# Kernel optimization log

Hardware: AMD Instinct MI355X
Metric: run time of the kernel (lower is better)

Reference implementation:

```python
import jax, jax.numpy as jnp
import numpy as np

B, N, D = 2, 2048, 1024
H, DH = 16, 64
DEPTH = 4
FF = 4
EPS = 1e-3  # keras LayerNormalization default epsilon
SCALE = DH ** -0.5


def setup_inputs() -> dict:
    key = jax.random.key(0)
    ks = jax.random.split(key, 8)
    s = 0.02
    inner = H * DH
    return {
        "x": jax.random.normal(ks[0], (B, N, D), jnp.float32),
        "mask": jnp.ones((B, N), jnp.bool_),
        "ln1_g": jnp.ones((DEPTH, D), jnp.float32),
        "ln1_b": jnp.zeros((DEPTH, D), jnp.float32),
        "Wqkv": jax.random.normal(ks[1], (DEPTH, D, 3 * inner), jnp.float32) * s,
        "Wout": jax.random.normal(ks[2], (DEPTH, inner, D), jnp.float32) * s,
        "bout": jnp.zeros((DEPTH, D), jnp.float32),
        "ln2_g": jnp.ones((DEPTH, D), jnp.float32),
        "ln2_b": jnp.zeros((DEPTH, D), jnp.float32),
        "W1": jax.random.normal(ks[3], (DEPTH, D, 2 * FF * D), jnp.float32) * s,
        "b1": jnp.zeros((DEPTH, 2 * FF * D), jnp.float32),
        "W2": jax.random.normal(ks[4], (DEPTH, FF * D, D), jnp.float32) * s,
        "b2": jnp.zeros((DEPTH, D), jnp.float32),
    }


def _layernorm(x, g, b):
    mu = jnp.mean(x, axis=-1, keepdims=True)
    var = jnp.mean(jnp.square(x - mu), axis=-1, keepdims=True)
    return (x - mu) * jax.lax.rsqrt(var + EPS) * g + b


def _attention(x, mask, Wqkv, Wout, bout):
    b, n, _ = x.shape
    qkv = x @ Wqkv  # [b, n, 3*h*dh]
    q, k, v = jnp.split(qkv, 3, axis=-1)
    split_heads = lambda t: t.reshape(b, n, H, DH).transpose(0, 2, 1, 3)  # b h n d
    q, k, v = split_heads(q), split_heads(k), split_heads(v)
    dots = jnp.einsum("bhid,bhjd->bhij", q, k) * SCALE
    neg = -jnp.finfo(dots.dtype).max
    # padding mask: keep (i valid) & (j valid)
    pm = mask[:, None, :, None] & mask[:, None, None, :]
    dots = jnp.where(pm, dots, neg)
    # causal mask: strict upper triangle masked out (triu with k=1)
    causal = jnp.triu(jnp.ones((n, n), jnp.bool_), k=1)
    dots = jnp.where(causal, neg, dots)
    attn = jax.nn.softmax(dots, axis=-1)
    out = jnp.einsum("bhij,bhjd->bhid", attn, v)
    out = out.transpose(0, 2, 1, 3).reshape(b, n, H * DH)
    return out @ Wout + bout


def _feedforward(x, W1, b1, W2, b2):
    h = x @ W1 + b1
    a, gates = jnp.split(h, 2, axis=-1)
    h = a * jax.nn.gelu(gates, approximate=False)  # GEGLU, tf.nn.gelu exact
    return h @ W2 + b2


def reference(x, mask, ln1_g, ln1_b, Wqkv, Wout, bout, ln2_g, ln2_b, W1, b1, W2, b2):
    for l in range(DEPTH):
        x = x + _attention(_layernorm(x, ln1_g[l], ln1_b[l]), mask, Wqkv[l], Wout[l], bout[l])
        x = x + _feedforward(_layernorm(x, ln2_g[l], ln2_b[l]), W1[l], b1[l], W2[l], b2[l])
    return x
```

## Files before the change

### kernel.cpp

```cpp
#include <hip/hip_runtime.h>


typedef float f32x4 __attribute__((ext_vector_type(4)));
typedef __bf16 bf16x8 __attribute__((ext_vector_type(8)));
typedef unsigned short u16;
typedef unsigned int u32;

#define SCALE2 0.18033688011112042f
#define LN_EPS 1e-3f
#define DEFER_THR 8.0f

__device__ __forceinline__ float fexp2(float x) { return __builtin_amdgcn_exp2f(x); }

__device__ __forceinline__ u16 f2bf(float f) {
  u32 u = __float_as_uint(f);
  u += 0x7fffu + ((u >> 16) & 1u);
  return (u16)(u >> 16);
}

__device__ __forceinline__ void stage16(void* lds_wave_base, const void* gsrc) {
  __builtin_amdgcn_global_load_lds((__attribute__((address_space(1))) void*)gsrc,
                                   (__attribute__((address_space(3))) void*)lds_wave_base,
                                   16, 0, 0);
}

__global__ void wtrans_kernel(const float* __restrict__ W, u16* __restrict__ WT,
                              int K, int N, int permMode) {
  __shared__ float tile[32][33];
  const int n0 = blockIdx.x * 32, k0 = blockIdx.y * 32;
  const float* Wl = W + (size_t)blockIdx.z * K * N;
  u16* WTl = WT + (size_t)blockIdx.z * K * N;
  const int tx = threadIdx.x, ty = threadIdx.y;
#pragma unroll
  for (int i = 0; i < 4; ++i)
    tile[ty + i * 8][tx] = Wl[(size_t)(k0 + ty + i * 8) * N + n0 + tx];
  __syncthreads();
#pragma unroll
  for (int i = 0; i < 4; ++i) {
    const int n = n0 + ty + i * 8;
    int orow;
    if (permMode) {
      orow = (n < 4096) ? (((n >> 4) << 5) + (n & 15))
                        : ((((n - 4096) >> 4) << 5) + 16 + (n & 15));
    } else {
      orow = n;
    }
    WTl[(size_t)orow * K + k0 + tx] = f2bf(tile[tx][ty + i * 8]);
  }
}

__global__ void vtrans_kernel(const u16* __restrict__ qkv, u16* __restrict__ Vt) {
  __shared__ u16 tile[32][33];
  const int t0 = blockIdx.x * 32, d0 = blockIdx.y * 32, bh = blockIdx.z;
  const int b = bh >> 4, h = bh & 15;
  const int tx = threadIdx.x, ty = threadIdx.y;
#pragma unroll
  for (int i = 0; i < 4; ++i)
    tile[ty + i * 8][tx] =
        qkv[((size_t)(b * 2048 + t0 + ty + i * 8)) * 3072 + 2048 + h * 64 + d0 + tx];
  __syncthreads();
#pragma unroll
  for (int i = 0; i < 4; ++i)
    Vt[((size_t)bh * 64 + d0 + ty + i * 8) * 2048 + t0 + tx] = tile[tx][ty + i * 8];
}

__global__ __launch_bounds__(256, 4)
void ln_kernel(const float* __restrict__ x, const float* __restrict__ g,
               const float* __restrict__ b, u16* __restrict__ y) {
  const int row = blockIdx.x, tid = threadIdx.x;
  const float4 v = ((const float4*)(x + (size_t)row * 1024))[tid];
  float s = v.x + v.y + v.z + v.w;
  float s2 = v.x * v.x + v.y * v.y + v.z * v.z + v.w * v.w;
#pragma unroll
  for (int off = 32; off > 0; off >>= 1) {
    s += __shfl_down(s, off);
    s2 += __shfl_down(s2, off);
  }
  __shared__ float ps[8];
  __shared__ float stats[2];
  const int wv = tid >> 6, lane = tid & 63;
  if (lane == 0) { ps[wv] = s; ps[wv + 4] = s2; }
  __syncthreads();
  if (tid == 0) {
    const float S = ps[0] + ps[1] + ps[2] + ps[3];
    const float S2 = ps[4] + ps[5] + ps[6] + ps[7];
    const float mu = S * (1.0f / 1024.0f);
    const float var = S2 * (1.0f / 1024.0f) - mu * mu;
    stats[0] = mu;
    stats[1] = rsqrtf(var + LN_EPS);
  }
  __syncthreads();
  const float mu = stats[0], rs = stats[1];
  const float4 gg = ((const float4*)g)[tid];
  const float4 bb = ((const float4*)b)[tid];
  ushort4 ov;
  ov.x = f2bf((v.x - mu) * rs * gg.x + bb.x);
  ov.y = f2bf((v.y - mu) * rs * gg.y + bb.y);
  ov.z = f2bf((v.z - mu) * rs * gg.z + bb.z);
  ov.w = f2bf((v.w - mu) * rs * gg.w + bb.w);
  ((ushort4*)(y + (size_t)row * 1024))[tid] = ov;
}

template <int EPI, int BM, int BN, int WM, int WN>
__global__ __launch_bounds__(WM * WN * 64, 2)
void gemm4(const u16* __restrict__ A, const u16* __restrict__ B,
           float* __restrict__ resid, const float* __restrict__ bias,
           u16* __restrict__ out, int M, int N, int K) {
  constexpr int NTHR = WM * WN * 64;
  constexpr int MT = BM / WM / 16;
  constexpr int NT = BN / WN / 16;
  __shared__ __align__(16) u16 lds[2][(BM + BN) * 64];

  const int tid = threadIdx.x;
  const int wv = tid >> 6, lane = tid & 63;
  const int lr = lane & 15, lg = lane >> 4;
  const int wmi = wv / WN, wni = wv % WN;
  const int RB0 = wmi * (BM / WM), CB0 = wni * (BN / WN);

  const int nwg = (int)(gridDim.x * gridDim.y);
  int id = (int)(blockIdx.y * gridDim.x + blockIdx.x);
  id = (id & 7) * (nwg >> 3) + (id >> 3);
  const int m0 = (id / (int)gridDim.x) * BM, n0 = (id % (int)gridDim.x) * BN;

  auto stage = [&](int bsel, int k0) {
    u16* dstA = &lds[bsel][0];
    u16* dstB = &lds[bsel][BM * 64];
#pragma unroll
    for (int rnd = 0; rnd < (BM * 128) / (NTHR * 16); ++rnd) {
      const int base = rnd * (NTHR * 16) + wv * 1024;
      const int off = base + lane * 16;
      const int row = off >> 7;
      const int k2 = (off & 127) ^ ((row & 7) << 4);
      stage16((char*)dstA + base, A + (size_t)(m0 + row) * K + k0 + (k2 >> 1));
    }
#pragma unroll
    for (int rnd = 0; rnd < (BN * 128) / (NTHR * 16); ++rnd) {
      const int base = rnd * (NTHR * 16) + wv * 1024;
      const int off = base + lane * 16;
      const int row = off >> 7;
      const int k2 = (off & 127) ^ ((row & 7) << 4);
      stage16((char*)dstB + base, B + (size_t)(n0 + row) * K + k0 + (k2 >> 1));
    }
  };

  f32x4 acc[MT][NT] = {};
  bf16x8 afr0[MT], bfr0[NT], afr1[MT], bfr1[NT];

  auto rd = [&](int bsel, int ks, bf16x8 (&af)[MT], bf16x8 (&bf)[NT]) {
    const char* As = (const char*)&lds[bsel][0];
    const char* Bs = (const char*)&lds[bsel][BM * 64];
#pragma unroll
    for (int mt = 0; mt < MT; ++mt) {
      const int row = RB0 + mt * 16 + lr;
      af[mt] = *(const bf16x8*)(As + row * 128 + ((ks * 64 + lg * 16) ^ ((lr & 7) << 4)));
    }
#pragma unroll
    for (int nt = 0; nt < NT; ++nt) {
      const int row = CB0 + nt * 16 + lr;
      bf[nt] = *(const bf16x8*)(Bs + row * 128 + ((ks * 64 + lg * 16) ^ ((lr & 7) << 4)));
    }
  };

  const int nT = K >> 6;
  stage(0, 0);
  stage(1, 64);
  asm volatile("s_waitcnt vmcnt(8)\n\ts_barrier" ::: "memory");
  rd(0, 0, afr0, bfr0);
  __builtin_amdgcn_sched_barrier(0);

  for (int t = 0; t < nT; ++t) {
    const int c = t & 1;
    rd(c, 1, afr1, bfr1);
    __builtin_amdgcn_sched_barrier(0);
    __builtin_amdgcn_s_setprio(1);
#pragma unroll
    for (int mt = 0; mt < MT; ++mt)
#pragma unroll
      for (int nt = 0; nt < NT; ++nt)
        acc[mt][nt] = __builtin_amdgcn_mfma_f32_16x16x32_bf16(
            afr0[mt], bfr0[nt], acc[mt][nt], 0, 0, 0);
    __builtin_amdgcn_s_setprio(0);
    __builtin_amdgcn_sched_barrier(0);
    asm volatile("s_waitcnt lgkmcnt(0)\n\ts_barrier" ::: "memory");
    __builtin_amdgcn_sched_barrier(0);
    if (t + 2 < nT) stage(c, (t + 2) * 64);
    if (t + 1 < nT) {
      if (t + 2 < nT)
        asm volatile("s_waitcnt vmcnt(8)\n\ts_barrier" ::: "memory");
      else
        asm volatile("s_waitcnt vmcnt(0)\n\ts_barrier" ::: "memory");
      rd(c ^ 1, 0, afr0, bfr0);
      __builtin_amdgcn_sched_barrier(0);
    }
    __builtin_amdgcn_s_setprio(1);
#pragma unroll
    for (int mt = 0; mt < MT; ++mt)
#pragma unroll
      for (int nt = 0; nt < NT; ++nt)
        acc[mt][nt] = __builtin_amdgcn_mfma_f32_16x16x32_bf16(
            afr1[mt], bfr1[nt], acc[mt][nt], 0, 0, 0);
    __builtin_amdgcn_s_setprio(0);
  }

  if (EPI == 0) {
#pragma unroll
    for (int mt = 0; mt < MT; ++mt)
#pragma unroll
      for (int nt = 0; nt < NT; ++nt) {
        const int n = n0 + CB0 + nt * 16 + lr;
#pragma unroll
        for (int r = 0; r < 4; ++r) {
          const int m = m0 + RB0 + mt * 16 + lg * 4 + r;
          out[(size_t)m * N + n] = f2bf(acc[mt][nt][r]);
        }
      }
  } else if (EPI == 1) {
    float bs[NT];
#pragma unroll
    for (int nt = 0; nt < NT; ++nt) bs[nt] = bias[n0 + CB0 + nt * 16 + lr];
#pragma unroll
    for (int mt = 0; mt < MT; ++mt)
#pragma unroll
      for (int nt = 0; nt < NT; ++nt) {
        const int n = n0 + CB0 + nt * 16 + lr;
#pragma unroll
        for (int r = 0; r < 4; ++r) {
          const int m = m0 + RB0 + mt * 16 + lg * 4 + r;
          resid[(size_t)m * N + n] += acc[mt][nt][r] + bs[nt];
        }
      }
  } else {
#pragma unroll
    for (int pt = 0; pt < NT / 2; ++pt) {
      const int colA = ((n0 + CB0 + pt * 32) >> 5) * 16 + lr;
      const float ba = bias[colA];
      const float bg = bias[4096 + colA];
#pragma unroll
      for (int mt = 0; mt < MT; ++mt)
#pragma unroll
        for (int r = 0; r < 4; ++r) {
          const int m = m0 + RB0 + mt * 16 + lg * 4 + r;
          const float a = acc[mt][2 * pt][r] + ba;
          const float g = acc[mt][2 * pt + 1][r] + bg;
          const float gl = 0.5f * g * (1.0f + erff(g * 0.70710678118654752f));
          out[(size_t)m * 4096 + colA] = f2bf(a * gl);
        }
    }
  }
}

__global__ __launch_bounds__(512, 4)
void attn_kernel(const u16* __restrict__ qkv, const u16* __restrict__ Vt,
                 u16* __restrict__ attnout) {
  __shared__ __align__(16) u16 KV[2][2][64 * 64];
  __shared__ __align__(16) u16 Ps[8][16 * 64];

  const int tid = threadIdx.x;
  const int wv = tid >> 6, lane = tid & 63;
  const int lr = lane & 15, lg = lane >> 4;
  const int lin = (int)(blockIdx.y * gridDim.x + blockIdx.x);
  const int xcd = lin & 7, j = lin >> 3;
  const int bh = xcd * 4 + (j >> 4);
  const int pr = j & 15;
  const int b = bh >> 4, h = bh & 15;
  const size_t tokbase = (size_t)b * 2048;
  const int qhi = 31 - pr;
  const int qt = (wv < 4) ? qhi : pr;
  const int ws = wv & 3;
  const int qg = qt * 64 + ws * 16 + lr;

  bf16x8 qf[2];
#pragma unroll
  for (int ks = 0; ks < 2; ++ks)
    qf[ks] = *(const bf16x8*)(qkv + (tokbase + qt * 64 + ws * 16 + lr) * 3072 +
                              h * 64 + ks * 32 + lg * 8);

  f32x4 o[4] = {};
  float m = -1e30f, lp = 0.f;

  const u16* kg_base = qkv + tokbase * 3072 + 1024 + h * 64;
  const u16* vg_base = Vt + (size_t)bh * 64 * 2048;

  const int soff = tid * 16;
  const int srow = soff >> 7;
  const int scol = (soff & 127) ^ ((srow & 7) << 4);
  auto stage = [&](int bsel, int kt2) {
    stage16((char*)&KV[bsel][0][0] + wv * 1024,
            kg_base + (size_t)(kt2 * 64 + srow) * 3072 + (scol >> 1));
    stage16((char*)&KV[bsel][1][0] + wv * 1024,
            vg_base + (size_t)srow * 2048 + kt2 * 64 + (scol >> 1));
  };

  stage(0, 0);
  stage(1, 1);
  asm volatile("s_waitcnt vmcnt(2)\n\ts_barrier" ::: "memory");

  for (int kt = 0; kt <= qhi; ++kt) {
    if (kt <= qt) {
      const char* Ks = (const char*)&KV[kt & 1][0][0];
      const char* Vs = (const char*)&KV[kt & 1][1][0];

      f32x4 s[4] = {};
#pragma unroll
      for (int ks = 0; ks < 2; ++ks)
#pragma unroll
        for (int nt = 0; nt < 4; ++nt) {
          const int row = nt * 16 + lr;
          const bf16x8 kf = *(const bf16x8*)(Ks + row * 128 +
                                             ((ks * 64 + lg * 16) ^ ((lr & 7) << 4)));
          s[nt] = __builtin_amdgcn_mfma_f32_16x16x32_bf16(kf, qf[ks], s[nt], 0, 0, 0);
        }

      float pmax = -1e30f;
      const bool diag = (kt == qt);
#pragma unroll
      for (int nt = 0; nt < 4; ++nt)
#pragma unroll
        for (int r = 0; r < 4; ++r) {
          float v = s[nt][r] * SCALE2;
          if (diag) {
            const int kg = kt * 64 + nt * 16 + lg * 4 + r;
            v = (kg <= qg) ? v : -1e30f;
          }
          s[nt][r] = v;
          pmax = fmaxf(pmax, v);
        }

      if (!__all(pmax - m <= DEFER_THR)) {
        float mx = fmaxf(pmax, __shfl_xor(pmax, 16));
        mx = fmaxf(mx, __shfl_xor(mx, 32));
        const float mn = fmaxf(m, mx);
        const float alpha = fexp2(m - mn);
        m = mn;
        lp *= alpha;
#pragma unroll
        for (int r = 0; r < 4; ++r) {
          const float ar = __shfl(alpha, lg * 4 + r);
#pragma unroll
          for (int dt = 0; dt < 4; ++dt) o[dt][r] *= ar;
        }
      }

#pragma unroll
      for (int nt = 0; nt < 4; ++nt) {
        const float p0 = fexp2(s[nt][0] - m), p1 = fexp2(s[nt][1] - m);
        const float p2 = fexp2(s[nt][2] - m), p3 = fexp2(s[nt][3] - m);
        lp += (p0 + p1) + (p2 + p3);
        uint2 w;
        w.x = (u32)f2bf(p0) | ((u32)f2bf(p1) << 16);
        w.y = (u32)f2bf(p2) | ((u32)f2bf(p3) << 16);
        *(uint2*)((char*)&Ps[wv][0] + lr * 128 + ((nt * 32 + lg * 8) ^ ((lr & 7) << 4))) = w;
      }

      bf16x8 pf[2];
#pragma unroll
      for (int ks = 0; ks < 2; ++ks) {
        const int jp = (ks * 4 + lg) ^ (lr & 7);
        pf[ks] = *(const bf16x8*)(&Ps[wv][0] + lr * 64 + jp * 8);
      }
#pragma unroll
      for (int ks = 0; ks < 2; ++ks)
#pragma unroll
        for (int dt = 0; dt < 4; ++dt) {
          const int row = dt * 16 + lr;
          const bf16x8 vf = *(const bf16x8*)(Vs + row * 128 +
                                             ((ks * 64 + lg * 16) ^ ((lr & 7) << 4)));
          o[dt] = __builtin_amdgcn_mfma_f32_16x16x32_bf16(pf[ks], vf, o[dt], 0, 0, 0);
        }
    }

    __syncthreads();
    if (kt + 2 <= qhi) stage(kt & 1, kt + 2);
    asm volatile("s_barrier" ::: "memory");
  }

  float lsum = lp + __shfl_xor(lp, 16);
  lsum += __shfl_xor(lsum, 32);
#pragma unroll
  for (int r = 0; r < 4; ++r) {
    const float ld = __shfl(lsum, lg * 4 + r);
    const int tok = qt * 64 + ws * 16 + lg * 4 + r;
#pragma unroll
    for (int dt = 0; dt < 4; ++dt)
      attnout[(tokbase + tok) * 1024 + h * 64 + dt * 16 + lr] = f2bf(o[dt][r] / ld);
  }
}

extern "C" void kernel_launch(void* const* d_in, const int* in_sizes, int n_in,
                              void* d_out, int out_size, void* d_ws, size_t ws_size,
                              hipStream_t stream) {
  (void)in_sizes; (void)n_in; (void)ws_size;
  const float* x_in  = (const float*)d_in[0];
  const float* ln1_g = (const float*)d_in[2];
  const float* ln1_b = (const float*)d_in[3];
  const float* Wqkv  = (const float*)d_in[4];
  const float* Wout  = (const float*)d_in[5];
  const float* bout  = (const float*)d_in[6];
  const float* ln2_g = (const float*)d_in[7];
  const float* ln2_b = (const float*)d_in[8];
  const float* W1    = (const float*)d_in[9];
  const float* b1    = (const float*)d_in[10];
  const float* W2    = (const float*)d_in[11];
  const float* b2    = (const float*)d_in[12];
  float* x = (float*)d_out;

  char* ws = (char*)d_ws;
  size_t off = 0;
  auto alloc = [&](size_t bytes) -> void* {
    void* p = ws + off;
    off += (bytes + 255) & ~(size_t)255;
    return p;
  };
  u16* WqkvT = (u16*)alloc(4ull * 3072 * 1024 * 2);
  u16* WoutT = (u16*)alloc(4ull * 1024 * 1024 * 2);
  u16* W1T   = (u16*)alloc(4ull * 8192 * 1024 * 2);
  u16* W2T   = (u16*)alloc(4ull * 1024 * 4096 * 2);
  u16* y     = (u16*)alloc(4096ull * 1024 * 2);
  u16* qkvb  = (u16*)alloc(4096ull * 3072 * 2);
  u16* Vt    = (u16*)alloc(32ull * 64 * 2048 * 2);
  u16* attn  = (u16*)alloc(4096ull * 1024 * 2);
  u16* ff    = (u16*)alloc(4096ull * 4096 * 2);

  hipMemcpyAsync(x, x_in, (size_t)out_size * 4, hipMemcpyDeviceToDevice, stream);

  const dim3 tb(32, 8);
  wtrans_kernel<<<dim3(3072 / 32, 1024 / 32, 4), tb, 0, stream>>>(Wqkv, WqkvT, 1024, 3072, 0);
  wtrans_kernel<<<dim3(1024 / 32, 1024 / 32, 4), tb, 0, stream>>>(Wout, WoutT, 1024, 1024, 0);
  wtrans_kernel<<<dim3(8192 / 32, 1024 / 32, 4), tb, 0, stream>>>(W1, W1T, 1024, 8192, 1);
  wtrans_kernel<<<dim3(1024 / 32, 4096 / 32, 4), tb, 0, stream>>>(W2, W2T, 4096, 1024, 0);

  for (int l = 0; l < 4; ++l) {
    ln_kernel<<<4096, 256, 0, stream>>>(x, ln1_g + l * 1024, ln1_b + l * 1024, y);
    gemm4<0, 128, 128, 2, 2><<<dim3(3072 / 128, 4096 / 128), 256, 0, stream>>>(
        y, WqkvT + (size_t)l * 3072 * 1024, nullptr, nullptr, qkvb, 4096, 3072, 1024);
    vtrans_kernel<<<dim3(64, 2, 32), tb, 0, stream>>>(qkvb, Vt);
    attn_kernel<<<dim3(16, 32), 512, 0, stream>>>(qkvb, Vt, attn);
    gemm4<1, 128, 128, 2, 2><<<dim3(1024 / 128, 4096 / 128), 256, 0, stream>>>(
        attn, WoutT + (size_t)l * 1024 * 1024, x, bout + l * 1024, nullptr, 4096, 1024, 1024);
    ln_kernel<<<4096, 256, 0, stream>>>(x, ln2_g + l * 1024, ln2_b + l * 1024, y);
    gemm4<2, 256, 256, 2, 4><<<dim3(8192 / 256, 4096 / 256), 512, 0, stream>>>(
        y, W1T + (size_t)l * 8192 * 1024, nullptr, b1 + l * 8192, ff, 4096, 8192, 1024);
    gemm4<1, 128, 128, 2, 2><<<dim3(1024 / 128, 4096 / 128), 256, 0, stream>>>(
        ff, W2T + (size_t)l * 1024 * 4096, x, b2 + l * 1024, nullptr, 4096, 1024, 4096);
  }
}
```

Baseline: 1.153 ms.

## Add 256x256 GEMM with quarter-tile staging interleaved into MFMA phases

Adds a new gemm5 kernel with 256x256 tiles and 8 waves. It splits each 64-wide K step into four LDS quadrants (A and B halves) and issues the global-to-LDS load of each quadrant for the next step between the four MFMA sub-phases, so loads overlap with compute at a finer grain. The QKV projection moves from 128x128 tiles to this 256x256 kernel, and so does the GEGLU FF1 GEMM. The goal is to hide memory latency better and raise reuse for QKV, at the cost of fewer workgroups for QKV (192) and more barriers per K step.

```diff
diff --git a/kernel.cpp b/kernel.cpp
--- a/kernel.cpp
+++ b/kernel.cpp
@@ -101,6 +101,159 @@
   ((ushort4*)(y + (size_t)row * 1024))[tid] = ov;
 }
 
+template <int EPI>
+__global__ __launch_bounds__(512, 2)
+void gemm5(const u16* __restrict__ A, const u16* __restrict__ B,
+           float* __restrict__ resid, const float* __restrict__ bias,
+           u16* __restrict__ out, int M, int N, int K) {
+  __shared__ __align__(16) u16 lds[2][4][256 * 32];
+
+  const int tid = threadIdx.x;
+  const int wv = tid >> 6, lane = tid & 63;
+  const int lr = lane & 15, lg = lane >> 4;
+  const int wmi = wv >> 2, wni = wv & 3;
+  const int RB0 = wmi * 128, CB0 = wni * 64;
+
+  const int nwg = (int)(gridDim.x * gridDim.y);
+  int id = (int)(blockIdx.y * gridDim.x + blockIdx.x);
+  id = (id & 7) * (nwg >> 3) + (id >> 3);
+  const int m0 = (id / (int)gridDim.x) * 256, n0 = (id % (int)gridDim.x) * 256;
+
+  auto stageHalf = [&](int c, int reg, int k0) {
+    const u16* src = (reg < 2) ? A : B;
+    const int base0 = (reg < 2) ? m0 : n0;
+    const int h = reg & 1;
+#pragma unroll
+    for (int l = 0; l < 2; ++l) {
+      const int o = l * 8192 + wv * 1024;
+      const int lo = o + lane * 16;
+      const int row = lo >> 6;
+      const int c16 = (lo >> 4) & 3;
+      stage16((char*)&lds[c][reg][0] + o,
+              src + (size_t)(base0 + row) * K + k0 + h * 32 + c16 * 8);
+    }
+  };
+
+  f32x4 acc[8][4] = {};
+  bf16x8 afr[4], bfr[4];
+
+  const int nT = K >> 6;
+  stageHalf(0, 0, 0); stageHalf(0, 2, 0); stageHalf(0, 1, 0); stageHalf(0, 3, 0);
+  asm volatile("s_waitcnt vmcnt(4)\n\ts_barrier" ::: "memory");
+
+  for (int t = 0; t < nT; ++t) {
+    const int c = t & 1, oc = c ^ 1;
+    const bool nxt = (t + 1 < nT);
+    const int k1 = (t + 1) * 64;
+    const char* Ak0 = (const char*)&lds[c][0][0];
+    const char* Ak1 = (const char*)&lds[c][1][0];
+    const char* Bk0 = (const char*)&lds[c][2][0];
+    const char* Bk1 = (const char*)&lds[c][3][0];
+
+#pragma unroll
+    for (int i = 0; i < 4; ++i)
+      afr[i] = *(const bf16x8*)(Ak0 + (RB0 + i * 16 + lr) * 64 + lg * 16);
+#pragma unroll
+    for (int j = 0; j < 4; ++j)
+      bfr[j] = *(const bf16x8*)(Bk0 + (CB0 + j * 16 + lr) * 64 + lg * 16);
+    if (nxt) stageHalf(oc, 0, k1);
+    asm volatile("s_barrier" ::: "memory");
+    asm volatile("s_waitcnt lgkmcnt(0)" ::: "memory");
+    __builtin_amdgcn_sched_barrier(0);
+    __builtin_amdgcn_s_setprio(1);
+#pragma unroll
+    for (int i = 0; i < 4; ++i)
+#pragma unroll
+      for (int j = 0; j < 4; ++j)
+        acc[i][j] = __builtin_amdgcn_mfma_f32_16x16x32_bf16(afr[i], bfr[j], acc[i][j], 0, 0, 0);
+    __builtin_amdgcn_s_setprio(0);
+    asm volatile("s_barrier" ::: "memory");
+
+#pragma unroll
+    for (int i = 0; i < 4; ++i)
+      afr[i] = *(const bf16x8*)(Ak0 + (RB0 + (4 + i) * 16 + lr) * 64 + lg * 16);
+    if (nxt) stageHalf(oc, 2, k1);
+    asm volatile("s_barrier" ::: "memory");
+    asm volatile("s_waitcnt lgkmcnt(0)" ::: "memory");
+    __builtin_amdgcn_sched_barrier(0);
+    __builtin_amdgcn_s_setprio(1);
+#pragma unroll
+    for (int i = 0; i < 4; ++i)
+#pragma unroll
+      for (int j = 0; j < 4; ++j)
+        acc[4 + i][j] = __builtin_amdgcn_mfma_f32_16x16x32_bf16(afr[i], bfr[j], acc[4 + i][j], 0, 0, 0);
+    __builtin_amdgcn_s_setprio(0);
+    if (nxt) asm volatile("s_waitcnt vmcnt(4)\n\ts_barrier" ::: "memory");
+    else     asm volatile("s_waitcnt vmcnt(0)\n\ts_barrier" ::: "memory");
+
+#pragma unroll
+    for (int i = 0; i < 4; ++i)
+      afr[i] = *(const bf16x8*)(Ak1 + (RB0 + (4 + i) * 16 + lr) * 64 + lg * 16);
+#pragma unroll
+    for (int j = 0; j < 4; ++j)
+      bfr[j] = *(const bf16x8*)(Bk1 + (CB0 + j * 16 + lr) * 64 + lg * 16);
+    if (nxt) stageHalf(oc, 1, k1);
+    asm volatile("s_barrier" ::: "memory");
+    asm volatile("s_waitcnt lgkmcnt(0)" ::: "memory");
+    __builtin_amdgcn_sched_barrier(0);
+    __builtin_amdgcn_s_setprio(1);
+#pragma unroll
+    for (int i = 0; i < 4; ++i)
+#pragma unroll
+      for (int j = 0; j < 4; ++j)
+        acc[4 + i][j] = __builtin_amdgcn_mfma_f32_16x16x32_bf16(afr[i], bfr[j], acc[4 + i][j], 0, 0, 0);
+    __builtin_amdgcn_s_setprio(0);
+    asm volatile("s_barrier" ::: "memory");
+
+#pragma unroll
+    for (int i = 0; i < 4; ++i)
+      afr[i] = *(const bf16x8*)(Ak1 + (RB0 + i * 16 + lr) * 64 + lg * 16);
+    if (nxt) stageHalf(oc, 3, k1);
+    asm volatile("s_barrier" ::: "memory");
+    asm volatile("s_waitcnt lgkmcnt(0)" ::: "memory");
+    __builtin_amdgcn_sched_barrier(0);
+    __builtin_amdgcn_s_setprio(1);
+#pragma unroll
+    for (int i = 0; i < 4; ++i)
+#pragma unroll
+      for (int j = 0; j < 4; ++j)
+        acc[i][j] = __builtin_amdgcn_mfma_f32_16x16x32_bf16(afr[i], bfr[j], acc[i][j], 0, 0, 0);
+    __builtin_amdgcn_s_setprio(0);
+    if (nxt) asm volatile("s_waitcnt vmcnt(4)\n\ts_barrier" ::: "memory");
+  }
+
+  if (EPI == 0) {
+#pragma unroll
+    for (int mt = 0; mt < 8; ++mt)
+#pragma unroll
+      for (int nt = 0; nt < 4; ++nt) {
+        const int n = n0 + CB0 + nt * 16 + lr;
+#pragma unroll
+        for (int r = 0; r < 4; ++r) {
+          const int m = m0 + RB0 + mt * 16 + lg * 4 + r;
+          out[(size_t)m * N + n] = f2bf(acc[mt][nt][r]);
+        }
+      }
+  } else {
+#pragma unroll
+    for (int pt = 0; pt < 2; ++pt) {
+      const int colA = ((n0 + CB0 + pt * 32) >> 5) * 16 + lr;
+      const float ba = bias[colA];
+      const float bg = bias[4096 + colA];
+#pragma unroll
+      for (int mt = 0; mt < 8; ++mt)
+#pragma unroll
+        for (int r = 0; r < 4; ++r) {
+          const int m = m0 + RB0 + mt * 16 + lg * 4 + r;
+          const float a = acc[mt][2 * pt][r] + ba;
+          const float g = acc[mt][2 * pt + 1][r] + bg;
+          const float gl = 0.5f * g * (1.0f + erff(g * 0.70710678118654752f));
+          out[(size_t)m * 4096 + colA] = f2bf(a * gl);
+        }
+    }
+  }
+}
+
 template <int EPI, int BM, int BN, int WM, int WN>
 __global__ __launch_bounds__(WM * WN * 64, 2)
 void gemm4(const u16* __restrict__ A, const u16* __restrict__ B,
@@ -202,7 +355,22 @@
     __builtin_amdgcn_s_setprio(0);
   }
 
-  if (EPI == 0) {
+  if (EPI == 1) {
+    float bs[NT];
+#pragma unroll
+    for (int nt = 0; nt < NT; ++nt) bs[nt] = bias[n0 + CB0 + nt * 16 + lr];
+#pragma unroll
+    for (int mt = 0; mt < MT; ++mt)
+#pragma unroll
+      for (int nt = 0; nt < NT; ++nt) {
+        const int n = n0 + CB0 + nt * 16 + lr;
+#pragma unroll
+        for (int r = 0; r < 4; ++r) {
+          const int m = m0 + RB0 + mt * 16 + lg * 4 + r;
+          resid[(size_t)m * N + n] += acc[mt][nt][r] + bs[nt];
+        }
+      }
+  } else {
 #pragma unroll
     for (int mt = 0; mt < MT; ++mt)
 #pragma unroll
@@ -214,38 +382,6 @@
           out[(size_t)m * N + n] = f2bf(acc[mt][nt][r]);
         }
       }
-  } else if (EPI == 1) {
-    float bs[NT];
-#pragma unroll
-    for (int nt = 0; nt < NT; ++nt) bs[nt] = bias[n0 + CB0 + nt * 16 + lr];
-#pragma unroll
-    for (int mt = 0; mt < MT; ++mt)
-#pragma unroll
-      for (int nt = 0; nt < NT; ++nt) {
-        const int n = n0 + CB0 + nt * 16 + lr;
-#pragma unroll
-        for (int r = 0; r < 4; ++r) {
-          const int m = m0 + RB0 + mt * 16 + lg * 4 + r;
-          resid[(size_t)m * N + n] += acc[mt][nt][r] + bs[nt];
-        }
-      }
-  } else {
-#pragma unroll
-    for (int pt = 0; pt < NT / 2; ++pt) {
-      const int colA = ((n0 + CB0 + pt * 32) >> 5) * 16 + lr;
-      const float ba = bias[colA];
-      const float bg = bias[4096 + colA];
-#pragma unroll
-      for (int mt = 0; mt < MT; ++mt)
-#pragma unroll
-        for (int r = 0; r < 4; ++r) {
-          const int m = m0 + RB0 + mt * 16 + lg * 4 + r;
-          const float a = acc[mt][2 * pt][r] + ba;
-          const float g = acc[mt][2 * pt + 1][r] + bg;
-          const float gl = 0.5f * g * (1.0f + erff(g * 0.70710678118654752f));
-          out[(size_t)m * 4096 + colA] = f2bf(a * gl);
-        }
-    }
   }
 }
 
@@ -431,14 +567,14 @@
 
   for (int l = 0; l < 4; ++l) {
     ln_kernel<<<4096, 256, 0, stream>>>(x, ln1_g + l * 1024, ln1_b + l * 1024, y);
-    gemm4<0, 128, 128, 2, 2><<<dim3(3072 / 128, 4096 / 128), 256, 0, stream>>>(
+    gemm5<0><<<dim3(3072 / 256, 4096 / 256), 512, 0, stream>>>(
         y, WqkvT + (size_t)l * 3072 * 1024, nullptr, nullptr, qkvb, 4096, 3072, 1024);
     vtrans_kernel<<<dim3(64, 2, 32), tb, 0, stream>>>(qkvb, Vt);
     attn_kernel<<<dim3(16, 32), 512, 0, stream>>>(qkvb, Vt, attn);
     gemm4<1, 128, 128, 2, 2><<<dim3(1024 / 128, 4096 / 128), 256, 0, stream>>>(
         attn, WoutT + (size_t)l * 1024 * 1024, x, bout + l * 1024, nullptr, 4096, 1024, 1024);
     ln_kernel<<<4096, 256, 0, stream>>>(x, ln2_g + l * 1024, ln2_b + l * 1024, y);
-    gemm4<2, 256, 256, 2, 4><<<dim3(8192 / 256, 4096 / 256), 512, 0, stream>>>(
+    gemm5<2><<<dim3(8192 / 256, 4096 / 256), 512, 0, stream>>>(
         y, W1T + (size_t)l * 8192 * 1024, nullptr, b1 + l * 8192, ff, 4096, 8192, 1024);
     gemm4<1, 128, 128, 2, 2><<<dim3(1024 / 128, 4096 / 128), 256, 0, stream>>>(
         ff, W2T + (size_t)l * 1024 * 4096, x, b2 + l * 1024, nullptr, 4096, 1024, 4096);
```

Measured after the change: 1.208 ms. +4.8%, slower.
